# Kernel optimization log

Hardware: AMD Instinct MI355X
Metric: run time of the kernel (lower is better)

The kernel has to match this reference:

```python
import jax, jax.numpy as jnp
import numpy as np

B, T, C, H = 2, 2048, 1024, 16
DH = C // H  # head_size = 64
EPS = 1e-5


def layernorm_axis1(x, gamma, beta):
    # Faithful to the torch code: mean/var over dim 1 (TIME axis), unbiased var.
    mean = jnp.mean(x, axis=1, keepdims=True)
    var = jnp.var(x, axis=1, ddof=1, keepdims=True)
    xhat = (x - mean) / jnp.sqrt(var + EPS)
    return gamma * xhat + beta


def setup_inputs() -> dict:
    key = jax.random.key(0)
    ks = jax.random.split(key, 16)
    s_in = 1.0 / np.sqrt(C)
    s_cat = 1.0 / np.sqrt(H * DH)
    s_ff = 1.0 / np.sqrt(4 * C)
    return {
        "x": jax.random.normal(ks[0], (B, T, C), dtype=jnp.float32),
        # per-head Q/K/V projections (no bias), stacked: [H, C, DH]
        "Wq": jax.random.uniform(ks[1], (H, C, DH), jnp.float32, -s_in, s_in),
        "Wk": jax.random.uniform(ks[2], (H, C, DH), jnp.float32, -s_in, s_in),
        "Wv": jax.random.uniform(ks[3], (H, C, DH), jnp.float32, -s_in, s_in),
        # attention output projection [H*DH, C] + bias
        "Wo": jax.random.uniform(ks[4], (H * DH, C), jnp.float32, -s_cat, s_cat),
        "bo": jax.random.uniform(ks[5], (C,), jnp.float32, -s_cat, s_cat),
        # FFN
        "W1": jax.random.uniform(ks[6], (C, 4 * C), jnp.float32, -s_in, s_in),
        "b1": jax.random.uniform(ks[7], (4 * C,), jnp.float32, -s_in, s_in),
        "W2": jax.random.uniform(ks[8], (4 * C, C), jnp.float32, -s_ff, s_ff),
        "b2": jax.random.uniform(ks[9], (C,), jnp.float32, -s_ff, s_ff),
        # LayerNorm affine params (plain tensors in the original)
        "gamma1": jnp.ones((C,), jnp.float32),
        "beta1": jnp.zeros((C,), jnp.float32),
        "gamma2": jnp.ones((C,), jnp.float32),
        "beta2": jnp.zeros((C,), jnp.float32),
    }


def reference(x, Wq, Wk, Wv, Wo, bo, W1, b1, W2, b2, gamma1, beta1, gamma2, beta2):
    # --- pre-LN attention sublayer ---
    x1 = layernorm_axis1(x, gamma1, beta1)                     # [B,T,C]
    q = jnp.einsum("btc,hcd->bhtd", x1, Wq)                    # [B,H,T,DH]
    k = jnp.einsum("btc,hcd->bhtd", x1, Wk)
    v = jnp.einsum("btc,hcd->bhtd", x1, Wv)
    # NOTE: scaled by full embedding dim C (not head_size) — faithful to source.
    scores = jnp.einsum("bhtd,bhsd->bhts", q, k) * (C ** -0.5)  # [B,H,T,T]
    causal = jnp.tril(jnp.ones((T, T), dtype=bool))
    scores = jnp.where(causal, scores, -jnp.inf)
    wei = jax.nn.softmax(scores, axis=-1)
    attn = jnp.einsum("bhts,bhsd->bhtd", wei, v)               # [B,H,T,DH]
    attn = attn.transpose(0, 2, 1, 3).reshape(B, T, H * DH)    # concat heads
    x = x + attn @ Wo + bo
    # --- pre-LN FFN sublayer ---
    x2 = layernorm_axis1(x, gamma2, beta2)
    h = jax.nn.relu(x2 @ W1 + b1)
    x = x + h @ W2 + b2
    return x
```

## Files before the change

### kernel.cpp

```cpp
#include <hip/hip_runtime.h>
#include <math.h>


#define TDIM 2048
#define BDIM 2
#define CDIM 1024
#define HDIM 16
#define DHE  64
#define QKVS 3072
#define NT   32
#define LNEPS 1e-5f
#define SC2  0.0450842200278f

typedef float f32x4 __attribute__((ext_vector_type(4)));
typedef __bf16 bf16x8 __attribute__((ext_vector_type(8)));
typedef __bf16 bf16x4 __attribute__((ext_vector_type(4)));

__device__ __forceinline__ void gld_lds16(const __bf16* g, __bf16* l) {
  __builtin_amdgcn_global_load_lds(
      (const __attribute__((address_space(1))) void*)g,
      (__attribute__((address_space(3))) void*)l, 16, 0, 0);
}

__global__ __launch_bounds__(256) void ln_stats(const float* __restrict__ x,
                                                float* __restrict__ sumv,
                                                float* __restrict__ sqv) {
  int c = blockIdx.x * 256 + threadIdx.x;
  int b = blockIdx.y;
  int t0 = blockIdx.z * (TDIM / 16);
  const float* xp = x + ((size_t)b * TDIM + t0) * CDIM + c;
  float s = 0.f, q = 0.f;
  for (int t = 0; t < TDIM / 16; ++t) {
    float v = xp[(size_t)t * CDIM];
    s += v;
    q += v * v;
  }
  atomicAdd(&sumv[b * CDIM + c], s);
  atomicAdd(&sqv[b * CDIM + c], q);
}

__global__ __launch_bounds__(256) void ln_apply(const float* __restrict__ x,
    const float* __restrict__ sumv, const float* __restrict__ sqv,
    const float* __restrict__ gamma, const float* __restrict__ beta,
    __bf16* __restrict__ y) {
  size_t i = (size_t)blockIdx.x * 256 + threadIdx.x;
  int c = (int)(i & (CDIM - 1));
  int b = (int)(i >> 21);
  float mean = sumv[b * CDIM + c] * (1.f / TDIM);
  float var = (sqv[b * CDIM + c] - mean * mean * (float)TDIM) * (1.f / (TDIM - 1));
  float rstd = rsqrtf(var + LNEPS);
  y[i] = (__bf16)(gamma[c] * (x[i] - mean) * rstd + beta[c]);
}

__global__ __launch_bounds__(256) void pack_all(
    const float* __restrict__ Wq, const float* __restrict__ Wk,
    const float* __restrict__ Wv, const float* __restrict__ Wo,
    const float* __restrict__ W1, const float* __restrict__ W2,
    __bf16* __restrict__ Wqkvb, __bf16* __restrict__ Wob,
    __bf16* __restrict__ W1b, __bf16* __restrict__ W2b) {
  __shared__ float tile[32][33];
  int t = blockIdx.x;
  int tx = threadIdx.x & 31, ty = threadIdx.x >> 5;
  if (t < 3072) {
    int mat = t >> 10, rem = t & 1023;
    int h = rem >> 6, rr = rem & 63;
    int c0 = (rr & 31) * 32, d0 = (rr >> 5) * 32;
    const float* W = (mat == 0) ? Wq : (mat == 1) ? Wk : Wv;
#pragma unroll
    for (int i = 0; i < 4; ++i)
      tile[ty + i * 8][tx] = W[((size_t)h * CDIM + c0 + ty + i * 8) * DHE + d0 + tx];
    __syncthreads();
#pragma unroll
    for (int i = 0; i < 4; ++i) {
      int n = mat * 1024 + h * 64 + d0 + ty + i * 8;
      Wqkvb[(size_t)n * CDIM + c0 + tx] = (__bf16)tile[tx][ty + i * 8];
    }
  } else {
    const float* in; __bf16* outp; int Cc, R, l;
    if (t < 4096)      { in = Wo; outp = Wob; R = 1024; Cc = 1024; l = t - 3072; }
    else if (t < 8192) { in = W1; outp = W1b; R = 1024; Cc = 4096; l = t - 4096; }
    else               { in = W2; outp = W2b; R = 4096; Cc = 1024; l = t - 8192; }
    int ncx = Cc >> 5;
    int c0 = (l % ncx) * 32, r0 = (l / ncx) * 32;
#pragma unroll
    for (int i = 0; i < 4; ++i)
      tile[ty + i * 8][tx] = in[(size_t)(r0 + ty + i * 8) * Cc + c0 + tx];
    __syncthreads();
#pragma unroll
    for (int i = 0; i < 4; ++i)
      outp[(size_t)(c0 + ty + i * 8) * R + r0 + tx] = (__bf16)tile[tx][ty + i * 8];
  }
}

__global__ __launch_bounds__(256) void transp_v(const __bf16* __restrict__ qkv,
    __bf16* __restrict__ vtb) {
  __shared__ __bf16 tile[32][33];
  int bh = blockIdx.y >> 1, d0 = (blockIdx.y & 1) * 32;
  int b = bh >> 4, h = bh & 15;
  int t0 = blockIdx.x * 32;
  int tx = threadIdx.x & 31, ty = threadIdx.x >> 5;
#pragma unroll
  for (int i = 0; i < 4; ++i)
    tile[ty + i * 8][tx] = qkv[((size_t)b * TDIM + t0 + ty + i * 8) * QKVS + 2048 + h * DHE + d0 + tx];
  __syncthreads();
#pragma unroll
  for (int i = 0; i < 4; ++i)
    vtb[((size_t)bh * 64 + d0 + ty + i * 8) * TDIM + t0 + tx] = tile[tx][ty + i * 8];
}

template<int BM, bool BIAS, bool RELU, bool OUTBF>
__global__ __launch_bounds__(BM * 2, (BM == 256) ? 4 : 3) void gemm_t(
    const __bf16* __restrict__ Ag, const __bf16* __restrict__ Bg,
    const float* __restrict__ bias, void* __restrict__ Cm,
    void* __restrict__ Cm2, void* __restrict__ Cm3, int msplit,
    int M, int N, int K, int ld, int gnx) {
  constexpr int T   = BM * 2;
  constexpr int PB  = (BM == 256) ? 1 : 2;
  constexpr int LPT = 2 + PB;
  constexpr int BUF = BM * 64 + 8192;
  __shared__ __align__(16) char lds[3 * BUF];

  int tid = threadIdx.x;
  int lane = tid & 63, wid = tid >> 6;
  int wm = wid >> 1, wn = wid & 1;
  int l15 = lane & 15, hi = lane >> 4;

  size_t koff = (size_t)blockIdx.y * K;
  Ag += koff; Bg += koff;

  int wgid = blockIdx.x;
  int m0 = (wgid / gnx) * BM, n0 = (wgid % gnx) * 128;
  void* Cuse = blockIdx.y ? (m0 < msplit ? Cm2 : Cm3) : Cm;

  int srow = tid >> 2;
  int skcol = ((tid & 3) ^ ((tid >> 3) & 3)) << 3;
  const int acS = ((hi ^ ((l15 >> 1) & 3)) << 4);

  f32x4 acc[4][4];
#pragma unroll
  for (int i = 0; i < 4; ++i)
#pragma unroll
    for (int j = 0; j < 4; ++j) acc[i][j] = (f32x4){0.f, 0.f, 0.f, 0.f};

  auto stageT = [&](int t) {
    char* dst = lds + (size_t)(t % 3) * BUF;
    int k0 = t << 5;
#pragma unroll
    for (int c = 0; c < 2; ++c)
      gld_lds16(Ag + (size_t)(m0 + c * (BM / 2) + srow) * ld + k0 + skcol,
                (__bf16*)(dst + c * (BM * 32)) + (size_t)tid * 8);
#pragma unroll
    for (int c = 0; c < PB; ++c)
      gld_lds16(Bg + (size_t)(n0 + c * (T / 4) + srow) * ld + k0 + skcol,
                (__bf16*)(dst + BM * 64 + c * (T * 16)) + (size_t)tid * 8);
  };

  int KT = K >> 5;
  stageT(0); stageT(1);
  if constexpr (BM == 256) asm volatile("s_waitcnt vmcnt(3)" ::: "memory");
  else                     asm volatile("s_waitcnt vmcnt(4)" ::: "memory");
  __builtin_amdgcn_s_barrier();

  bf16x8 a[4], b[4];
  for (int t = 0; t < KT; ++t) {
    if (t + 2 < KT) stageT(t + 2);
    const char* buf = lds + (size_t)(t % 3) * BUF;
#pragma unroll
    for (int i = 0; i < 4; ++i)
      a[i] = *(const bf16x8*)(buf + (wm * 64 + i * 16 + l15) * 64 + acS);
#pragma unroll
    for (int j = 0; j < 4; ++j)
      b[j] = *(const bf16x8*)(buf + BM * 64 + (wn * 64 + j * 16 + l15) * 64 + acS);
    __builtin_amdgcn_s_setprio(1);
#pragma unroll
    for (int i = 0; i < 4; ++i)
#pragma unroll
      for (int j = 0; j < 4; ++j)
        acc[i][j] = __builtin_amdgcn_mfma_f32_16x16x32_bf16(a[i], b[j], acc[i][j], 0, 0, 0);
    __builtin_amdgcn_s_setprio(0);
    if (t + 1 < KT) {
      asm volatile("" ::: "memory");
      if (t + 2 < KT) {
        if constexpr (BM == 256) asm volatile("s_waitcnt vmcnt(3)" ::: "memory");
        else                     asm volatile("s_waitcnt vmcnt(4)" ::: "memory");
      } else {
        asm volatile("s_waitcnt vmcnt(0)" ::: "memory");
      }
      __builtin_amdgcn_s_barrier();
    }
  }

#pragma unroll
  for (int fm = 0; fm < 4; ++fm) {
    int row = m0 + wm * 64 + fm * 16 + hi * 4;
#pragma unroll
    for (int fn = 0; fn < 4; ++fn) {
      int col = n0 + wn * 64 + fn * 16 + l15;
#pragma unroll
      for (int j = 0; j < 4; ++j) {
        float v = acc[fm][fn][j];
        size_t off = (size_t)(row + j) * N + col;
        if (BIAS) v += bias[col];
        if (RELU) v = fmaxf(v, 0.f);
        if (OUTBF) ((__bf16*)Cuse)[off] = (__bf16)v;
        else       ((float*)Cuse)[off] = v;
      }
    }
  }
}

__global__ __launch_bounds__(256) void splitk_reduce(const float* __restrict__ p0,
    const float* __restrict__ p1a, const float* __restrict__ p1b, int msplit,
    const float* __restrict__ bias, const float* __restrict__ res,
    float* __restrict__ out) {
  size_t i = ((size_t)blockIdx.x * 256 + threadIdx.x) * 4;
  int c = (int)(i & (CDIM - 1));
  int row = (int)(i >> 10);
  const float* p1 = (row < msplit) ? p1a : p1b;
  float4 a = *(const float4*)(p0 + i);
  float4 b = *(const float4*)(p1 + i);
  float4 r = *(const float4*)(res + i);
  float4 bb = *(const float4*)(bias + c);
  float4 v;
  v.x = a.x + b.x + r.x + bb.x;
  v.y = a.y + b.y + r.y + bb.y;
  v.z = a.z + b.z + r.z + bb.z;
  v.w = a.w + b.w + r.w + bb.w;
  *(float4*)(out + i) = v;
}

__global__ __launch_bounds__(256) void wo_reduce_ln(const float* __restrict__ q0,
    const float* __restrict__ q1, const float* __restrict__ bo,
    const float* __restrict__ x, float* __restrict__ xmid,
    float* __restrict__ sumv, float* __restrict__ sqv) {
  int c = blockIdx.x * 256 + threadIdx.x;
  int b = blockIdx.y;
  int t0 = blockIdx.z * (TDIM / 16);
  size_t base = ((size_t)b * TDIM + t0) * CDIM + c;
  float bb = bo[c];
  float s = 0.f, q = 0.f;
  for (int t = 0; t < TDIM / 16; ++t) {
    size_t i = base + (size_t)t * CDIM;
    float v = q0[i] + q1[i] + bb + x[i];
    xmid[i] = v;
    s += v;
    q += v * v;
  }
  atomicAdd(&sumv[b * CDIM + c], s);
  atomicAdd(&sqv[b * CDIM + c], q);
}

__global__ __launch_bounds__(512, 4) void attn_mfma(const __bf16* __restrict__ qkv,
    const __bf16* __restrict__ vt, __bf16* __restrict__ o) {
  __shared__ __align__(16) char smem[55296];
  __bf16 (*Ks)[64][72] = (__bf16 (*)[64][72])(smem);
  __bf16 (*Vs)[64][72] = (__bf16 (*)[64][72])(smem + 18432);
  __bf16 (*Ps)[16][72] = (__bf16 (*)[16][72])(smem + 36864);
  float (*Os)[64]      = (float (*)[64])(smem);
  float* ms = (float*)(smem + 16384);
  float* ls = (float*)(smem + 16640);

  int bh = blockIdx.y;
  int b = bh >> 4, h = bh & 15;
  int bxA = blockIdx.x;
  int bxB = NT - 1 - bxA;
  int tid = threadIdx.x;
  int lane = tid & 63, w = tid >> 6;
  int wq = w & 3;
  int g = w >> 2;
  int l15 = lane & 15, hi = lane >> 4;
  int hi4 = hi * 4;
  size_t bT = (size_t)b * TDIM;

  bf16x8 onesb;
#pragma unroll
  for (int i = 0; i < 8; ++i) onesb[i] = (l15 == 0) ? (__bf16)1.0f : (__bf16)0.0f;

  bf16x8 qfA[2], qfB[2];
  {
    const __bf16* qp = qkv + (bT + bxA * 64 + wq * 16 + l15) * QKVS + h * DHE;
    qfA[0] = *(const bf16x8*)(qp + hi * 8);
    qfA[1] = *(const bf16x8*)(qp + 32 + hi * 8);
    qp = qkv + (bT + bxB * 64 + wq * 16 + l15) * QKVS + h * DHE;
    qfB[0] = *(const bf16x8*)(qp + hi * 8);
    qfB[1] = *(const bf16x8*)(qp + 32 + hi * 8);
  }

  float mA = -INFINITY, mB = -INFINITY;
  f32x4 lA = (f32x4){0.f, 0.f, 0.f, 0.f};
  f32x4 lB = (f32x4){0.f, 0.f, 0.f, 0.f};
  f32x4 oA[4], oB[4];
#pragma unroll
  for (int n = 0; n < 4; ++n) {
    oA[n] = (f32x4){0.f, 0.f, 0.f, 0.f};
    oB[n] = (f32x4){0.f, 0.f, 0.f, 0.f};
  }

  int g_tid = tid & 255;
  int r0 = g_tid >> 3, c8 = (g_tid & 7) * 8;

  auto process = [&](const bf16x8* qf, float& m_i, f32x4& l_acc, f32x4* oacc,
                     int bx, int t2) {
    f32x4 sacc[4];
#pragma unroll
    for (int n = 0; n < 4; ++n) sacc[n] = (f32x4){0.f, 0.f, 0.f, 0.f};
    __builtin_amdgcn_s_setprio(1);
#pragma unroll
    for (int n = 0; n < 4; ++n)
#pragma unroll
      for (int kk = 0; kk < 2; ++kk) {
        bf16x8 kf = *(const bf16x8*)&Ks[g][n * 16 + l15][kk * 32 + hi * 8];
        sacc[n] = __builtin_amdgcn_mfma_f32_16x16x32_bf16(kf, qf[kk], sacc[n], 0, 0, 0);
      }
    __builtin_amdgcn_s_setprio(0);

    int myq = wq * 16 + l15;
    if (t2 == bx) {
#pragma unroll
      for (int n = 0; n < 4; ++n)
#pragma unroll
        for (int j = 0; j < 4; ++j)
          if (n * 16 + hi4 + j > myq) sacc[n][j] = -INFINITY;
    }

    float mx = sacc[0][0];
#pragma unroll
    for (int n = 0; n < 4; ++n) {
      float a0 = fmaxf(sacc[n][0], sacc[n][1]);
      float a1 = fmaxf(sacc[n][2], sacc[n][3]);
      mx = fmaxf(mx, fmaxf(a0, a1));
    }
    mx = fmaxf(mx, __shfl_xor(mx, 16));
    mx = fmaxf(mx, __shfl_xor(mx, 32));
    mx *= SC2;

    if (!__all(mx - m_i <= 8.0f)) {
      float nm = fmaxf(m_i, mx);
      float al = exp2f(m_i - nm);
      m_i = nm;
#pragma unroll
      for (int r = 0; r < 4; ++r) {
        float ao = __shfl(al, hi4 + r);
        l_acc[r] *= ao;
#pragma unroll
        for (int n = 0; n < 4; ++n) oacc[n][r] *= ao;
      }
    }

    float negm = -m_i;
#pragma unroll
    for (int n = 0; n < 4; ++n) {
      bf16x4 pv;
#pragma unroll
      for (int j = 0; j < 4; ++j)
        pv[j] = (__bf16)exp2f(fmaf(sacc[n][j], SC2, negm));
      *(bf16x4*)&Ps[w][l15][n * 16 + hi4] = pv;
    }

    bf16x8 pa0 = *(const bf16x8*)&Ps[w][l15][hi * 8];
    bf16x8 pa1 = *(const bf16x8*)&Ps[w][l15][32 + hi * 8];
    __builtin_amdgcn_s_setprio(1);
#pragma unroll
    for (int n = 0; n < 4; ++n) {
      bf16x8 vf0 = *(const bf16x8*)&Vs[g][n * 16 + l15][hi * 8];
      bf16x8 vf1 = *(const bf16x8*)&Vs[g][n * 16 + l15][32 + hi * 8];
      oacc[n] = __builtin_amdgcn_mfma_f32_16x16x32_bf16(pa0, vf0, oacc[n], 0, 0, 0);
      oacc[n] = __builtin_amdgcn_mfma_f32_16x16x32_bf16(pa1, vf1, oacc[n], 0, 0, 0);
    }
    l_acc = __builtin_amdgcn_mfma_f32_16x16x32_bf16(pa0, onesb, l_acc, 0, 0, 0);
    l_acc = __builtin_amdgcn_mfma_f32_16x16x32_bf16(pa1, onesb, l_acc, 0, 0, 0);
    __builtin_amdgcn_s_setprio(0);
  };

  for (int j = 0; j <= bxB / 2; ++j) {
    int t2 = 2 * j + g;
    bool have = (t2 <= bxB);
    __syncthreads();
    if (have) {
#pragma unroll
      for (int rr = 0; rr < 2; ++rr) {
        int row = rr * 32 + r0;
        *(bf16x8*)&Ks[g][row][c8] =
            *(const bf16x8*)(qkv + (bT + t2 * 64 + row) * QKVS + 1024 + h * DHE + c8);
        *(bf16x8*)&Vs[g][row][c8] =
            *(const bf16x8*)(vt + ((size_t)bh * 64 + row) * TDIM + t2 * 64 + c8);
      }
    }
    __syncthreads();
    if (t2 <= bxA) process(qfA, mA, lA, oA, bxA, t2);
    if (have)      process(qfB, mB, lB, oB, bxB, t2);
  }

  auto merge = [&](int bx, float m_i, const f32x4& l_acc, f32x4* oacc) {
    float m_o[4], l_o[4];
#pragma unroll
    for (int r = 0; r < 4; ++r) {
      m_o[r] = __shfl(m_i, hi4 + r);
      l_o[r] = __shfl(l_acc[r], lane & 48);
    }
    __syncthreads();
    if (g == 1) {
#pragma unroll
      for (int r = 0; r < 4; ++r) {
        int lrow = wq * 16 + hi4 + r;
        if (l15 == 0) { ms[lrow] = m_o[r]; ls[lrow] = l_o[r]; }
#pragma unroll
        for (int n = 0; n < 4; ++n)
          Os[lrow][n * 16 + l15] = oacc[n][r];
      }
    }
    __syncthreads();
    if (g == 0) {
#pragma unroll
      for (int r = 0; r < 4; ++r) {
        int lrow = wq * 16 + hi4 + r;
        float m1 = ms[lrow], l1 = ls[lrow];
        float mm = fmaxf(m_o[r], m1);
        float e0 = exp2f(m_o[r] - mm), e1 = exp2f(m1 - mm);
        float inv = 1.f / (l_o[r] * e0 + l1 * e1);
        size_t row = bT + bx * 64 + lrow;
#pragma unroll
        for (int n = 0; n < 4; ++n) {
          float v = (oacc[n][r] * e0 + Os[lrow][n * 16 + l15] * e1) * inv;
          o[row * CDIM + h * DHE + n * 16 + l15] = (__bf16)v;
        }
      }
    }
  };
  merge(bxA, mA, lA, oA);
  merge(bxB, mB, lB, oB);
}

extern "C" void kernel_launch(void* const* d_in, const int* in_sizes, int n_in,
                              void* d_out, int out_size, void* d_ws, size_t ws_size,
                              hipStream_t stream) {
  (void)in_sizes; (void)n_in; (void)out_size; (void)ws_size;
  const float* x   = (const float*)d_in[0];
  const float* Wq  = (const float*)d_in[1];
  const float* Wk  = (const float*)d_in[2];
  const float* Wv  = (const float*)d_in[3];
  const float* Wo  = (const float*)d_in[4];
  const float* bo  = (const float*)d_in[5];
  const float* W1  = (const float*)d_in[6];
  const float* b1  = (const float*)d_in[7];
  const float* W2  = (const float*)d_in[8];
  const float* b2  = (const float*)d_in[9];
  const float* g1  = (const float*)d_in[10];
  const float* be1 = (const float*)d_in[11];
  const float* g2  = (const float*)d_in[12];
  const float* be2 = (const float*)d_in[13];
  float* out = (float*)d_out;

  char* wsb = (char*)d_ws;
  const size_t MB = 1024 * 1024;
  __bf16* Wqkvb = (__bf16*)(wsb + 0);
  __bf16* Wob   = (__bf16*)(wsb + 6  * MB);
  __bf16* W1b   = (__bf16*)(wsb + 8  * MB);
  __bf16* W2b   = (__bf16*)(wsb + 16 * MB);
  __bf16* qkvb  = (__bf16*)(wsb + 24 * MB);
  __bf16* hb    = (__bf16*)(wsb + 24 * MB);
  __bf16* vtb   = (__bf16*)(wsb + 48 * MB);
  __bf16* x1b   = (__bf16*)(wsb + 56 * MB);
  __bf16* attnb = (__bf16*)(wsb + 56 * MB);
  float*  xmid  = (float*) (wsb + 64 * MB);
  __bf16* x2b   = (__bf16*)(wsb + 80 * MB);
  float*  stats = (float*) (wsb + 88 * MB);
  float*  q0    = (float*) (wsb + 24 * MB);
  float*  q1    = (float*) (wsb + 40 * MB);
  float*  p0    = (float*) (wsb + 0);
  float*  p1a   = (float*) (wsb + 56 * MB);
  float*  p1b   = (float*) (wsb + 80 * MB) - 2048 * 1024;
  float* sum1 = stats,        *sq1 = stats + 2048;
  float* sum2 = stats + 4096, *sq2 = stats + 6144;

  hipMemsetAsync(stats, 0, 4 * 2048 * sizeof(float), stream);

  pack_all<<<dim3(12288), 256, 0, stream>>>(Wq, Wk, Wv, Wo, W1, W2,
                                            Wqkvb, Wob, W1b, W2b);

  ln_stats<<<dim3(CDIM / 256, BDIM, 16), 256, 0, stream>>>(x, sum1, sq1);
  ln_apply<<<dim3((BDIM * TDIM * CDIM) / 256), 256, 0, stream>>>(x, sum1, sq1, g1, be1, x1b);

  gemm_t<256, false, false, true><<<dim3(384, 1), 512, 0, stream>>>(
      x1b, Wqkvb, nullptr, qkvb, qkvb, qkvb, 0, 4096, 3072, 1024, 1024, 24);

  transp_v<<<dim3(TDIM / 32, 64), 256, 0, stream>>>(qkvb, vtb);

  attn_mfma<<<dim3(NT / 2, BDIM * HDIM), 512, 0, stream>>>(qkvb, vtb, attnb);

  gemm_t<128, false, false, false><<<dim3(256, 2), 256, 0, stream>>>(
      attnb, Wob, nullptr, q0, q1, q1, 4096, 4096, 1024, 512, 1024, 8);
  wo_reduce_ln<<<dim3(CDIM / 256, BDIM, 16), 256, 0, stream>>>(
      q0, q1, bo, x, xmid, sum2, sq2);

  ln_apply<<<dim3((BDIM * TDIM * CDIM) / 256), 256, 0, stream>>>(xmid, sum2, sq2, g2, be2, x2b);

  gemm_t<256, true, true, true><<<dim3(512, 1), 512, 0, stream>>>(
      x2b, W1b, b1, hb, hb, hb, 0, 4096, 4096, 1024, 1024, 32);

  gemm_t<128, false, false, false><<<dim3(256, 2), 256, 0, stream>>>(
      hb, W2b, nullptr, p0, p1a, p1b, 2048, 4096, 1024, 2048, 4096, 8);
  splitk_reduce<<<dim3(4096), 256, 0, stream>>>(p0, p1a, p1b, 2048, b2, xmid, out);
}
```

Before: 260.9 us.

## Replace split-K GEMMs with BN=64 tiles and fused bias/residual epilogues

The Wo and W2 GEMMs no longer split K across two partial buffers. Each now uses 128x64 tiles with 512 workgroups and adds bias and residual directly in the epilogue. This removes the splitk_reduce and wo_reduce_ln passes and their extra fp32 partial-buffer traffic, but a separate ln_stats pass over xmid is now needed. The attention kernel also prefetches the next K/V tile into registers while the current tile is processed, hiding global load latency at the cost of extra registers.

```diff
diff --git a/kernel.cpp b/kernel.cpp
--- a/kernel.cpp
+++ b/kernel.cpp
@@ -108,16 +108,15 @@
     vtb[((size_t)bh * 64 + d0 + ty + i * 8) * TDIM + t0 + tx] = tile[tx][ty + i * 8];
 }
 
-template<int BM, bool BIAS, bool RELU, bool OUTBF>
-__global__ __launch_bounds__(BM * 2, (BM == 256) ? 4 : 3) void gemm_t(
+template<int BM, int BN, bool BIAS, bool RES, bool RELU, bool OUTBF>
+__global__ __launch_bounds__(BM * 2, 4) void gemm_t(
     const __bf16* __restrict__ Ag, const __bf16* __restrict__ Bg,
-    const float* __restrict__ bias, void* __restrict__ Cm,
-    void* __restrict__ Cm2, void* __restrict__ Cm3, int msplit,
-    int M, int N, int K, int ld, int gnx) {
+    const float* __restrict__ bias, const float* __restrict__ res,
+    void* __restrict__ Cm, int M, int N, int K, int ld, int gnx) {
   constexpr int T   = BM * 2;
-  constexpr int PB  = (BM == 256) ? 1 : 2;
-  constexpr int LPT = 2 + PB;
-  constexpr int BUF = BM * 64 + 8192;
+  constexpr int WN  = BN / 2;
+  constexpr int FN  = WN / 16;
+  constexpr int BUF = (BM + BN) * 64;
   __shared__ __align__(16) char lds[3 * BUF];
 
   int tid = threadIdx.x;
@@ -125,22 +124,18 @@
   int wm = wid >> 1, wn = wid & 1;
   int l15 = lane & 15, hi = lane >> 4;
 
-  size_t koff = (size_t)blockIdx.y * K;
-  Ag += koff; Bg += koff;
-
   int wgid = blockIdx.x;
-  int m0 = (wgid / gnx) * BM, n0 = (wgid % gnx) * 128;
-  void* Cuse = blockIdx.y ? (m0 < msplit ? Cm2 : Cm3) : Cm;
+  int m0 = (wgid / gnx) * BM, n0 = (wgid % gnx) * BN;
 
   int srow = tid >> 2;
   int skcol = ((tid & 3) ^ ((tid >> 3) & 3)) << 3;
   const int acS = ((hi ^ ((l15 >> 1) & 3)) << 4);
 
-  f32x4 acc[4][4];
+  f32x4 acc[4][FN];
 #pragma unroll
   for (int i = 0; i < 4; ++i)
 #pragma unroll
-    for (int j = 0; j < 4; ++j) acc[i][j] = (f32x4){0.f, 0.f, 0.f, 0.f};
+    for (int j = 0; j < FN; ++j) acc[i][j] = (f32x4){0.f, 0.f, 0.f, 0.f};
 
   auto stageT = [&](int t) {
     char* dst = lds + (size_t)(t % 3) * BUF;
@@ -149,19 +144,16 @@
     for (int c = 0; c < 2; ++c)
       gld_lds16(Ag + (size_t)(m0 + c * (BM / 2) + srow) * ld + k0 + skcol,
                 (__bf16*)(dst + c * (BM * 32)) + (size_t)tid * 8);
-#pragma unroll
-    for (int c = 0; c < PB; ++c)
-      gld_lds16(Bg + (size_t)(n0 + c * (T / 4) + srow) * ld + k0 + skcol,
-                (__bf16*)(dst + BM * 64 + c * (T * 16)) + (size_t)tid * 8);
+    gld_lds16(Bg + (size_t)(n0 + srow) * ld + k0 + skcol,
+              (__bf16*)(dst + BM * 64) + (size_t)tid * 8);
   };
 
   int KT = K >> 5;
   stageT(0); stageT(1);
-  if constexpr (BM == 256) asm volatile("s_waitcnt vmcnt(3)" ::: "memory");
-  else                     asm volatile("s_waitcnt vmcnt(4)" ::: "memory");
+  asm volatile("s_waitcnt vmcnt(3)" ::: "memory");
   __builtin_amdgcn_s_barrier();
 
-  bf16x8 a[4], b[4];
+  bf16x8 a[4], b[FN];
   for (int t = 0; t < KT; ++t) {
     if (t + 2 < KT) stageT(t + 2);
     const char* buf = lds + (size_t)(t % 3) * BUF;
@@ -169,23 +161,19 @@
     for (int i = 0; i < 4; ++i)
       a[i] = *(const bf16x8*)(buf + (wm * 64 + i * 16 + l15) * 64 + acS);
 #pragma unroll
-    for (int j = 0; j < 4; ++j)
-      b[j] = *(const bf16x8*)(buf + BM * 64 + (wn * 64 + j * 16 + l15) * 64 + acS);
+    for (int j = 0; j < FN; ++j)
+      b[j] = *(const bf16x8*)(buf + BM * 64 + (wn * WN + j * 16 + l15) * 64 + acS);
     __builtin_amdgcn_s_setprio(1);
 #pragma unroll
     for (int i = 0; i < 4; ++i)
 #pragma unroll
-      for (int j = 0; j < 4; ++j)
+      for (int j = 0; j < FN; ++j)
         acc[i][j] = __builtin_amdgcn_mfma_f32_16x16x32_bf16(a[i], b[j], acc[i][j], 0, 0, 0);
     __builtin_amdgcn_s_setprio(0);
     if (t + 1 < KT) {
       asm volatile("" ::: "memory");
-      if (t + 2 < KT) {
-        if constexpr (BM == 256) asm volatile("s_waitcnt vmcnt(3)" ::: "memory");
-        else                     asm volatile("s_waitcnt vmcnt(4)" ::: "memory");
-      } else {
-        asm volatile("s_waitcnt vmcnt(0)" ::: "memory");
-      }
+      if (t + 2 < KT) asm volatile("s_waitcnt vmcnt(3)" ::: "memory");
+      else            asm volatile("s_waitcnt vmcnt(0)" ::: "memory");
       __builtin_amdgcn_s_barrier();
     }
   }
@@ -194,60 +182,20 @@
   for (int fm = 0; fm < 4; ++fm) {
     int row = m0 + wm * 64 + fm * 16 + hi * 4;
 #pragma unroll
-    for (int fn = 0; fn < 4; ++fn) {
-      int col = n0 + wn * 64 + fn * 16 + l15;
+    for (int fn = 0; fn < FN; ++fn) {
+      int col = n0 + wn * WN + fn * 16 + l15;
 #pragma unroll
       for (int j = 0; j < 4; ++j) {
         float v = acc[fm][fn][j];
         size_t off = (size_t)(row + j) * N + col;
         if (BIAS) v += bias[col];
+        if (RES)  v += res[off];
         if (RELU) v = fmaxf(v, 0.f);
-        if (OUTBF) ((__bf16*)Cuse)[off] = (__bf16)v;
-        else       ((float*)Cuse)[off] = v;
-      }
-    }
-  }
-}
-
-__global__ __launch_bounds__(256) void splitk_reduce(const float* __restrict__ p0,
-    const float* __restrict__ p1a, const float* __restrict__ p1b, int msplit,
-    const float* __restrict__ bias, const float* __restrict__ res,
-    float* __restrict__ out) {
-  size_t i = ((size_t)blockIdx.x * 256 + threadIdx.x) * 4;
-  int c = (int)(i & (CDIM - 1));
-  int row = (int)(i >> 10);
-  const float* p1 = (row < msplit) ? p1a : p1b;
-  float4 a = *(const float4*)(p0 + i);
-  float4 b = *(const float4*)(p1 + i);
-  float4 r = *(const float4*)(res + i);
-  float4 bb = *(const float4*)(bias + c);
-  float4 v;
-  v.x = a.x + b.x + r.x + bb.x;
-  v.y = a.y + b.y + r.y + bb.y;
-  v.z = a.z + b.z + r.z + bb.z;
-  v.w = a.w + b.w + r.w + bb.w;
-  *(float4*)(out + i) = v;
-}
-
-__global__ __launch_bounds__(256) void wo_reduce_ln(const float* __restrict__ q0,
-    const float* __restrict__ q1, const float* __restrict__ bo,
-    const float* __restrict__ x, float* __restrict__ xmid,
-    float* __restrict__ sumv, float* __restrict__ sqv) {
-  int c = blockIdx.x * 256 + threadIdx.x;
-  int b = blockIdx.y;
-  int t0 = blockIdx.z * (TDIM / 16);
-  size_t base = ((size_t)b * TDIM + t0) * CDIM + c;
-  float bb = bo[c];
-  float s = 0.f, q = 0.f;
-  for (int t = 0; t < TDIM / 16; ++t) {
-    size_t i = base + (size_t)t * CDIM;
-    float v = q0[i] + q1[i] + bb + x[i];
-    xmid[i] = v;
-    s += v;
-    q += v * v;
-  }
-  atomicAdd(&sumv[b * CDIM + c], s);
-  atomicAdd(&sqv[b * CDIM + c], q);
+        if (OUTBF) ((__bf16*)Cm)[off] = (__bf16)v;
+        else       ((float*)Cm)[off] = v;
+      }
+    }
+  }
 }
 
 __global__ __launch_bounds__(512, 4) void attn_mfma(const __bf16* __restrict__ qkv,
@@ -372,6 +320,14 @@
     __builtin_amdgcn_s_setprio(0);
   };
 
+  bf16x8 kr[2], vr[2];
+#pragma unroll
+  for (int rr = 0; rr < 2; ++rr) {
+    int row = rr * 32 + r0;
+    kr[rr] = *(const bf16x8*)(qkv + (bT + g * 64 + row) * QKVS + 1024 + h * DHE + c8);
+    vr[rr] = *(const bf16x8*)(vt + ((size_t)bh * 64 + row) * TDIM + g * 64 + c8);
+  }
+
   for (int j = 0; j <= bxB / 2; ++j) {
     int t2 = 2 * j + g;
     bool have = (t2 <= bxB);
@@ -380,13 +336,20 @@
 #pragma unroll
       for (int rr = 0; rr < 2; ++rr) {
         int row = rr * 32 + r0;
-        *(bf16x8*)&Ks[g][row][c8] =
-            *(const bf16x8*)(qkv + (bT + t2 * 64 + row) * QKVS + 1024 + h * DHE + c8);
-        *(bf16x8*)&Vs[g][row][c8] =
-            *(const bf16x8*)(vt + ((size_t)bh * 64 + row) * TDIM + t2 * 64 + c8);
-      }
-    }
-    __syncthreads();
+        *(bf16x8*)&Ks[g][row][c8] = kr[rr];
+        *(bf16x8*)&Vs[g][row][c8] = vr[rr];
+      }
+    }
+    __syncthreads();
+    int t2n = t2 + 2;
+    if (t2n <= bxB) {
+#pragma unroll
+      for (int rr = 0; rr < 2; ++rr) {
+        int row = rr * 32 + r0;
+        kr[rr] = *(const bf16x8*)(qkv + (bT + t2n * 64 + row) * QKVS + 1024 + h * DHE + c8);
+        vr[rr] = *(const bf16x8*)(vt + ((size_t)bh * 64 + row) * TDIM + t2n * 64 + c8);
+      }
+    }
     if (t2 <= bxA) process(qfA, mA, lA, oA, bxA, t2);
     if (have)      process(qfB, mB, lB, oB, bxB, t2);
   }
@@ -465,11 +428,6 @@
   float*  xmid  = (float*) (wsb + 64 * MB);
   __bf16* x2b   = (__bf16*)(wsb + 80 * MB);
   float*  stats = (float*) (wsb + 88 * MB);
-  float*  q0    = (float*) (wsb + 24 * MB);
-  float*  q1    = (float*) (wsb + 40 * MB);
-  float*  p0    = (float*) (wsb + 0);
-  float*  p1a   = (float*) (wsb + 56 * MB);
-  float*  p1b   = (float*) (wsb + 80 * MB) - 2048 * 1024;
   float* sum1 = stats,        *sq1 = stats + 2048;
   float* sum2 = stats + 4096, *sq2 = stats + 6144;
 
@@ -481,24 +439,22 @@
   ln_stats<<<dim3(CDIM / 256, BDIM, 16), 256, 0, stream>>>(x, sum1, sq1);
   ln_apply<<<dim3((BDIM * TDIM * CDIM) / 256), 256, 0, stream>>>(x, sum1, sq1, g1, be1, x1b);
 
-  gemm_t<256, false, false, true><<<dim3(384, 1), 512, 0, stream>>>(
-      x1b, Wqkvb, nullptr, qkvb, qkvb, qkvb, 0, 4096, 3072, 1024, 1024, 24);
+  gemm_t<256, 128, false, false, false, true><<<dim3(384), 512, 0, stream>>>(
+      x1b, Wqkvb, nullptr, nullptr, qkvb, 4096, 3072, 1024, 1024, 24);
 
   transp_v<<<dim3(TDIM / 32, 64), 256, 0, stream>>>(qkvb, vtb);
 
   attn_mfma<<<dim3(NT / 2, BDIM * HDIM), 512, 0, stream>>>(qkvb, vtb, attnb);
 
-  gemm_t<128, false, false, false><<<dim3(256, 2), 256, 0, stream>>>(
-      attnb, Wob, nullptr, q0, q1, q1, 4096, 4096, 1024, 512, 1024, 8);
-  wo_reduce_ln<<<dim3(CDIM / 256, BDIM, 16), 256, 0, stream>>>(
-      q0, q1, bo, x, xmid, sum2, sq2);
-
+  gemm_t<128, 64, true, true, false, false><<<dim3(512), 256, 0, stream>>>(
+      attnb, Wob, bo, x, xmid, 4096, 1024, 1024, 1024, 16);
+
+  ln_stats<<<dim3(CDIM / 256, BDIM, 16), 256, 0, stream>>>(xmid, sum2, sq2);
   ln_apply<<<dim3((BDIM * TDIM * CDIM) / 256), 256, 0, stream>>>(xmid, sum2, sq2, g2, be2, x2b);
 
-  gemm_t<256, true, true, true><<<dim3(512, 1), 512, 0, stream>>>(
-      x2b, W1b, b1, hb, hb, hb, 0, 4096, 4096, 1024, 1024, 32);
-
-  gemm_t<128, false, false, false><<<dim3(256, 2), 256, 0, stream>>>(
-      hb, W2b, nullptr, p0, p1a, p1b, 2048, 4096, 1024, 2048, 4096, 8);
-  splitk_reduce<<<dim3(4096), 256, 0, stream>>>(p0, p1a, p1b, 2048, b2, xmid, out);
-}
+  gemm_t<256, 128, true, false, true, true><<<dim3(512), 512, 0, stream>>>(
+      x2b, W1b, b1, nullptr, hb, 4096, 4096, 1024, 1024, 32);
+
+  gemm_t<128, 64, true, true, false, false><<<dim3(512), 256, 0, stream>>>(
+      hb, W2b, b2, xmid, out, 4096, 1024, 4096, 4096, 16);
+}
```

Measured after the change: 250.0 us. -4.2%, faster.
